# Performance work log

Measured on AMD Instinct MI355X. Metric: run time of the kernel, lower is better.

Reference implementation:

```python
import jax, jax.numpy as jnp
import numpy as np

EPS_SUM = 1e-8
EPS_FILL = 1e-4
NORM_THRESH = 0.1
MASK_THRESH = 0.1


def _shift1(x):
    # conv2d with 1x3 filter [1,1,0], padding (0,1): out[i] = x[i-1] + x[i]
    return x + jnp.pad(x, ((0, 0), (0, 0), (0, 0), (1, 0)))[..., :-1]


def _shift2(x):
    # conv2d with 1x3 filter [0,1,1], padding (0,1): out[i] = x[i] + x[i+1]
    return x + jnp.pad(x, ((0, 0), (0, 0), (0, 0), (0, 1)))[..., 1:]


def _fill(disp, vm, shift_fn, n_steps):
    # Hole filling: each step propagates valid disparity one pixel; after W
    # steps the data-dependent while-loop of the original has converged
    # (further steps are identity), so a fixed-length scan is equivalent.
    def step(carry, _):
        d, m = carry
        m1 = shift_fn(m)
        nm = (m1 > 0).astype(d.dtype)
        d = d * m + shift_fn(d) / (m1 + EPS_FILL) * (nm - m)
        return (d, nm), None
    (disp, vm), _ = jax.lax.scan(step, (disp, vm), None, length=n_steps)
    return disp, vm


def regress_disp(att, valid_mask):
    # att: [B,H,W,W], valid_mask: [B,1,H,W]
    b, h, w, _ = att.shape
    idx = jnp.arange(w, dtype=att.dtype)
    disp_ini = idx[None, None, None, :] - jnp.sum(att * idx, axis=-1).reshape(b, 1, h, w)
    disp = disp_ini * valid_mask
    disp, vm = _fill(disp, valid_mask, _shift1, w)  # left-to-right pass
    disp, vm = _fill(disp, vm, _shift2, w)          # right-to-left pass
    return disp_ini * valid_mask + disp * (1.0 - valid_mask)


def masked_exp_norm(cost, lower):
    # tril/triu-masked exp normalization (non-standard attention)
    tri = jnp.tril if lower else jnp.triu
    c = tri(cost)
    c = jnp.exp(c - jnp.max(c, axis=-1, keepdims=True))
    c = tri(c)
    return c / (jnp.sum(c, axis=-1, keepdims=True) + EPS_SUM)


def gen_pos_shift(w, dtype):
    p = jnp.linspace(0.0, 2.0, w).astype(dtype)
    pos = jnp.maximum(p[:, None] - p[None, :], 0.0)  # pos_l - pos_r, clipped
    return pos[None, None]  # [1,1,W,W]


def gen_raw_disp(att, pos_shift):
    hi = jnp.argmax(att, axis=-1)
    rr = jnp.stack([hi - 1, hi, hi + 1], axis=-1) + 1  # indices into padded axis
    att_pad = jnp.pad(att, ((0, 0), (0, 0), (0, 0), (1, 1)))
    aw = jnp.take_along_axis(att_pad, rr, axis=-1)
    norm = jnp.sum(aw, axis=-1, keepdims=True)
    norm = jnp.where(norm < NORM_THRESH, 1.0, norm)
    aw = aw / norm
    pos_pad = jnp.broadcast_to(jnp.pad(pos_shift, ((0, 0), (0, 0), (0, 0), (1, 1))), att_pad.shape)
    pr = jnp.take_along_axis(pos_pad, rr, axis=-1)
    return jnp.sum(aw * pr, axis=-1)  # [B,H,W]


def setup_inputs() -> dict:
    key = jax.random.key(0)
    k1, k2 = jax.random.split(key)
    B, H, W = 1, 64, 512
    cost1 = jax.random.normal(k1, (B, H, W, W), dtype=jnp.float32)
    cost2 = jax.random.normal(k2, (B, H, W, W), dtype=jnp.float32)
    return {"cost1": cost1, "cost2": cost2}


def reference(cost1, cost2):
    b, h, w, _ = cost1.shape
    att_r2l = masked_exp_norm(cost2, lower=True)   # right-to-left attention
    att_l2r = masked_exp_norm(cost1, lower=False)  # left-to-right attention
    vm_left = (jnp.sum(att_l2r, axis=-2) > MASK_THRESH).astype(cost1.dtype).reshape(b, 1, h, w)
    vm_right = (jnp.sum(att_r2l, axis=-2) > MASK_THRESH).astype(cost1.dtype).reshape(b, 1, h, w)
    disp_r2l = regress_disp(att_r2l, vm_left)   # [B,1,H,W]
    disp_l2r = regress_disp(att_l2r, vm_right)  # [B,1,H,W]
    pos = gen_pos_shift(w, cost1.dtype)
    raw_l2r = gen_raw_disp(att_r2l, pos)                               # [B,H,W]
    raw_r2l = gen_raw_disp(att_l2r, jnp.swapaxes(pos, -1, -2))         # [B,H,W]
    return jnp.concatenate([disp_r2l, disp_l2r, raw_l2r[:, None], raw_r2l[:, None]], axis=1)
```

## Files before the change

kernel.cpp:

```cpp
#include <hip/hip_runtime.h>
#include <float.h>

#define H 64
#define W 512
#define SPLIT 8

template<bool LOWER, bool FULLROW>
__device__ __forceinline__ void process_rows(
    const float* __restrict__ hb, const int h, const int s,
    const int lane, const int wid,
    float* __restrict__ disp, float* __restrict__ raw, float* scol)
{
  constexpr int NH = FULLROW ? 2 : 1;
  constexpr int JB = FULLROW ? 0 : (LOWER ? 0 : 256);
  const float pscale = 2.0f / 511.0f;

  float cacc[NH * 4];
  #pragma unroll
  for (int q = 0; q < NH * 4; q++) cacc[q] = 0.f;

  int   jmap[NH * 4];
  float jfmap[NH * 4];
  #pragma unroll
  for (int hh = 0; hh < NH; hh++)
    #pragma unroll
    for (int k = 0; k < 4; k++) {
      jmap[hh * 4 + k]  = JB + hh * 256 + lane * 4 + k;
      jfmap[hh * 4 + k] = (float)jmap[hh * 4 + k];
    }

  for (int t = wid; t < 64; t += 8) {
    const int i = s * 64 + t;
    const float fi = (float)i;
    const float* rp = hb + (size_t)i * W;

    float c[NH * 4];
    #pragma unroll
    for (int hh = 0; hh < NH; hh++) {
      const float4 v = ((const float4*)rp)[(JB >> 2) + hh * 64 + lane];
      c[hh*4+0] = v.x; c[hh*4+1] = v.y; c[hh*4+2] = v.z; c[hh*4+3] = v.w;
    }

    float best = -FLT_MAX;
    int   bj   = 1024;
    #pragma unroll
    for (int hh = 0; hh < NH; hh++) {
      const bool NM = FULLROW ? (LOWER ? (hh == 1) : (hh == 0)) : true;
      #pragma unroll
      for (int k = 0; k < 4; k++) {
        const int q = hh * 4 + k;
        float v = c[q];
        if (NM) {
          const bool vld = LOWER ? (jmap[q] <= i) : (jmap[q] >= i);
          v = vld ? v : -FLT_MAX;
          c[q] = v;
        }
        if (v > best) { best = v; bj = jmap[q]; }
      }
    }
    #pragma unroll
    for (int off = 32; off; off >>= 1) {
      const float ov = __shfl_xor(best, off);
      const int   oj = __shfl_xor(bj, off);
      if (ov > best || (ov == best && oj < bj)) { best = ov; bj = oj; }
    }

    const int bjm = bj - 1, bjp = bj + 1;
    const int am = min(max(bjm, 0), W - 1);
    const int ap = min(bjp, W - 1);
    const float cm_ = rp[am];
    const float cp_ = rp[ap];

    const bool hasMasked = LOWER ? (i < W - 1) : (i > 0);
    const float mx = hasMasked ? fmaxf(best, 0.f) : best;

    float ssum = 0.f, wsum = 0.f;
    #pragma unroll
    for (int q = 0; q < NH * 4; q++) {
      const float e = __expf(c[q] - mx);
      c[q] = e;
      ssum += e;
      wsum = fmaf(e, jfmap[q], wsum);
    }
    #pragma unroll
    for (int off = 32; off; off >>= 1) {
      ssum += __shfl_xor(ssum, off);
      wsum += __shfl_xor(wsum, off);
    }
    const float inv = 1.f / (ssum + 1e-8f);

    #pragma unroll
    for (int q = 0; q < NH * 4; q++) cacc[q] = fmaf(c[q], inv, cacc[q]);

    if (lane == 0) {
      const bool pv = LOWER ? (bjm >= 0) : (bjm >= i);
      const bool nv = LOWER ? (bjp <= i) : (bjp <= W - 1);
      const float e_h = __expf(best - mx);
      const float e_p = pv ? __expf(cm_ - mx) : 0.f;
      const float e_n = nv ? __expf(cp_ - mx) : 0.f;
      const float t0 = e_p + e_h + e_n;
      const float w0 = fmaf(e_p, (float)bjm, fmaf(e_h, (float)bj, e_n * (float)bjp));
      disp[h * W + i] = fi - wsum * inv;
      const float n0 = t0 * inv;
      const float t1 = pscale * (LOWER ? (fi * t0 - w0) : (w0 - fi * t0));
      raw[h * W + i] = (t1 * inv) / (n0 < 0.1f ? 1.f : n0);
    }
  }

  #pragma unroll
  for (int q = 0; q < NH * 4; q++) atomicAdd(&scol[jmap[q]], cacc[q]);
}

__global__ __launch_bounds__(512) void attn_stats_all(
    const float* __restrict__ cost1, const float* __restrict__ cost2,
    float* __restrict__ disp_r2l, float* __restrict__ disp_l2r,
    float* __restrict__ cs_r2l,  float* __restrict__ cs_l2r,
    float* __restrict__ out)
{
  __shared__ float scol[W];
  const int tid  = threadIdx.x;
  const int lane = tid & 63;
  const int wid  = tid >> 6;
  const int gid  = blockIdx.x;
  const bool lower = (gid & 1) == 0;
  const int rest = gid >> 1;
  const int h    = rest >> 3;
  const int s    = rest & 7;

  const float* cost = lower ? cost2 : cost1;
  float* disp = lower ? disp_r2l : disp_l2r;
  float* csum = lower ? cs_r2l  : cs_l2r;
  float* raw  = out + (lower ? 2 : 3) * (H * W);
  const float* hb = cost + (size_t)h * W * W;

  scol[tid] = 0.f;
  __syncthreads();

  if (lower) {
    if (s < 4) process_rows<true,  false>(hb, h, s, lane, wid, disp, raw, scol);
    else       process_rows<true,  true >(hb, h, s, lane, wid, disp, raw, scol);
  } else {
    if (s < 4) process_rows<false, true >(hb, h, s, lane, wid, disp, raw, scol);
    else       process_rows<false, false>(hb, h, s, lane, wid, disp, raw, scol);
  }
  __syncthreads();

  const bool doMine = lower ? (s >= 4 || tid < 256)
                            : (s < 4  || tid >= 256);
  if (doMine) atomicAdd(&csum[h * W + tid], scol[tid]);
}

__global__ __launch_bounds__(64) void fill_rows(
    const float* __restrict__ dispA, const float* __restrict__ csA,
    const float* __restrict__ dispB, const float* __restrict__ csB,
    float* __restrict__ out)
{
  __shared__ float xrow[W];
  const int pair = blockIdx.x >> 6;
  const int h    = blockIdx.x & 63;
  const float* dsp = (pair ? dispB : dispA) + h * W;
  const float* cs  = (pair ? csB  : csA ) + h * W;
  float* o = out + pair * (H * W) + h * W;
  const int lane = threadIdx.x;
  const int j0 = lane * 8;

  float x[8];
  bool m[8];
  int incl[8];
  int run = -1, fv = W;
  #pragma unroll
  for (int k = 0; k < 8; k++) {
    x[k] = dsp[j0 + k];
    m[k] = cs[j0 + k] > 0.1f;
    xrow[j0 + k] = x[k];
    if (m[k]) { run = j0 + k; if (fv == W) fv = j0 + k; }
    incl[k] = run;
  }
  int v = run;
  #pragma unroll
  for (int off = 1; off < 64; off <<= 1) {
    const int tv = __shfl_up(v, off);
    if (lane >= off) v = max(v, tv);
  }
  int excl = __shfl_up(v, 1);
  if (lane == 0) excl = -1;
  int p0 = fv;
  #pragma unroll
  for (int off = 32; off; off >>= 1) p0 = min(p0, __shfl_xor(p0, off));
  __syncthreads();

  const float C2 = -1.4426229e-4f;
  #pragma unroll
  for (int k = 0; k < 8; k++) {
    const int jj = j0 + k;
    float ov;
    if (m[k]) {
      ov = x[k];
    } else {
      const int p = max(excl, incl[k]);
      if (p >= 0)        ov = xrow[p]  * exp2f(C2 * (float)(jj - p));
      else if (p0 < W)   ov = xrow[p0] * exp2f(C2 * (float)(p0 - jj));
      else               ov = 0.f;
    }
    o[jj] = ov;
  }
}

extern "C" void kernel_launch(void* const* d_in, const int* in_sizes, int n_in,
                              void* d_out, int out_size, void* d_ws, size_t ws_size,
                              hipStream_t stream) {
  const float* cost1 = (const float*)d_in[0];
  const float* cost2 = (const float*)d_in[1];
  float* out = (float*)d_out;
  float* w = (float*)d_ws;
  float* disp_r2l_ini = w;
  float* disp_l2r_ini = w + 32768;
  float* cs_l2r       = w + 65536;
  float* cs_r2l       = w + 98304;

  hipMemsetAsync(cs_l2r, 0, 2 * (size_t)H * W * sizeof(float), stream);

  attn_stats_all<<<2 * H * SPLIT, 512, 0, stream>>>(
      cost1, cost2, disp_r2l_ini, disp_l2r_ini, cs_r2l, cs_l2r, out);

  fill_rows<<<2 * H, 64, 0, stream>>>(disp_r2l_ini, cs_l2r,
                                      disp_l2r_ini, cs_r2l, out);
}
```

Before: 162.2 us.

## Use DPP wave reductions, register neighbor gather, and double block split

Replaces the shuffle-based argmax and sum reductions with DPP row/broadcast steps plus readlane, which avoids LDS-backed cross-lane traffic. The two neighbor values of the argmax are now taken from the already-computed exponentials in registers via readlane, so the dependent global loads and extra exps are gone. It also doubles the row split per image row (SPLIT 16, 32 rows per block) to launch more blocks. In exchange, more blocks each issue their own column-sum atomics, and the select chain adds ALU work.

```diff
diff --git a/kernel.cpp b/kernel.cpp
--- a/kernel.cpp
+++ b/kernel.cpp
@@ -3,7 +3,42 @@
 
 #define H 64
 #define W 512
-#define SPLIT 8
+#define SPLIT 16
+
+
+template<int C>
+__device__ __forceinline__ float dppf(float idv, float v) {
+  return __int_as_float(__builtin_amdgcn_update_dpp(
+      __float_as_int(idv), __float_as_int(v), C, 0xF, 0xF, false));
+}
+template<int C>
+__device__ __forceinline__ int dppi(int idv, int v) {
+  return __builtin_amdgcn_update_dpp(idv, v, C, 0xF, 0xF, false);
+}
+
+__device__ __forceinline__ void argmax_reduce64(float& b, int& j) {
+#define AR_STEP(C) { const float ob = dppf<C>(-FLT_MAX, b); \
+                     const int   oj = dppi<C>(1024, j); \
+                     if (ob > b || (ob == b && oj < j)) { b = ob; j = oj; } }
+  AR_STEP(0x111)
+  AR_STEP(0x112)
+  AR_STEP(0x114)
+  AR_STEP(0x118)
+  AR_STEP(0x142)
+  AR_STEP(0x143)
+#undef AR_STEP
+  b = __int_as_float(__builtin_amdgcn_readlane(__float_as_int(b), 63));
+  j = __builtin_amdgcn_readlane(j, 63);
+}
+
+__device__ __forceinline__ void sum2_reduce64(float& a, float& w) {
+#define S_STEP(C) { a += dppf<C>(0.f, a); w += dppf<C>(0.f, w); }
+  S_STEP(0x111) S_STEP(0x112) S_STEP(0x114) S_STEP(0x118)
+  S_STEP(0x142) S_STEP(0x143)
+#undef S_STEP
+  a = __int_as_float(__builtin_amdgcn_readlane(__float_as_int(a), 63));
+  w = __int_as_float(__builtin_amdgcn_readlane(__float_as_int(w), 63));
+}
 
 template<bool LOWER, bool FULLROW>
 __device__ __forceinline__ void process_rows(
@@ -29,8 +64,8 @@
       jfmap[hh * 4 + k] = (float)jmap[hh * 4 + k];
     }
 
-  for (int t = wid; t < 64; t += 8) {
-    const int i = s * 64 + t;
+  for (int t = wid; t < 32; t += 8) {
+    const int i = s * 32 + t;
     const float fi = (float)i;
     const float* rp = hb + (size_t)i * W;
 
@@ -58,18 +93,7 @@
         if (v > best) { best = v; bj = jmap[q]; }
       }
     }
-    #pragma unroll
-    for (int off = 32; off; off >>= 1) {
-      const float ov = __shfl_xor(best, off);
-      const int   oj = __shfl_xor(bj, off);
-      if (ov > best || (ov == best && oj < bj)) { best = ov; bj = oj; }
-    }
-
-    const int bjm = bj - 1, bjp = bj + 1;
-    const int am = min(max(bjm, 0), W - 1);
-    const int ap = min(bjp, W - 1);
-    const float cm_ = rp[am];
-    const float cp_ = rp[ap];
+    argmax_reduce64(best, bj);
 
     const bool hasMasked = LOWER ? (i < W - 1) : (i > 0);
     const float mx = hasMasked ? fmaxf(best, 0.f) : best;
@@ -82,22 +106,41 @@
       ssum += e;
       wsum = fmaf(e, jfmap[q], wsum);
     }
-    #pragma unroll
-    for (int off = 32; off; off >>= 1) {
-      ssum += __shfl_xor(ssum, off);
-      wsum += __shfl_xor(wsum, off);
-    }
+    sum2_reduce64(ssum, wsum);
     const float inv = 1.f / (ssum + 1e-8f);
 
     #pragma unroll
     for (int q = 0; q < NH * 4; q++) cacc[q] = fmaf(c[q], inv, cacc[q]);
 
+    const int bjm = bj - 1, bjp = bj + 1;
+    const bool pv = LOWER ? (bjm >= 0) : (bjm >= i);
+    const bool nv = LOWER ? (bjp <= i) : (bjp <= W - 1);
+    float e_p = 0.f, e_n = 0.f;
+    {
+      const int jcl = min(max(bjm, JB), JB + NH * 256 - 1);
+      const int rsel = ((jcl - JB) >> 8) * 4 + (jcl & 3);
+      const int lsel = ((jcl - JB) >> 2) & 63;
+      float sel = c[0];
+      #pragma unroll
+      for (int q = 1; q < NH * 4; q++) sel = (rsel == q) ? c[q] : sel;
+      const float g = __int_as_float(
+          __builtin_amdgcn_readlane(__float_as_int(sel), lsel));
+      e_p = pv ? g : 0.f;
+    }
+    {
+      const int jcl = min(max(bjp, JB), JB + NH * 256 - 1);
+      const int rsel = ((jcl - JB) >> 8) * 4 + (jcl & 3);
+      const int lsel = ((jcl - JB) >> 2) & 63;
+      float sel = c[0];
+      #pragma unroll
+      for (int q = 1; q < NH * 4; q++) sel = (rsel == q) ? c[q] : sel;
+      const float g = __int_as_float(
+          __builtin_amdgcn_readlane(__float_as_int(sel), lsel));
+      e_n = nv ? g : 0.f;
+    }
+
     if (lane == 0) {
-      const bool pv = LOWER ? (bjm >= 0) : (bjm >= i);
-      const bool nv = LOWER ? (bjp <= i) : (bjp <= W - 1);
       const float e_h = __expf(best - mx);
-      const float e_p = pv ? __expf(cm_ - mx) : 0.f;
-      const float e_n = nv ? __expf(cp_ - mx) : 0.f;
       const float t0 = e_p + e_h + e_n;
       const float w0 = fmaf(e_p, (float)bjm, fmaf(e_h, (float)bj, e_n * (float)bjp));
       disp[h * W + i] = fi - wsum * inv;
@@ -124,8 +167,8 @@
   const int gid  = blockIdx.x;
   const bool lower = (gid & 1) == 0;
   const int rest = gid >> 1;
-  const int h    = rest >> 3;
-  const int s    = rest & 7;
+  const int h    = rest >> 4;
+  const int s    = rest & 15;
 
   const float* cost = lower ? cost2 : cost1;
   float* disp = lower ? disp_r2l : disp_l2r;
@@ -137,16 +180,16 @@
   __syncthreads();
 
   if (lower) {
-    if (s < 4) process_rows<true,  false>(hb, h, s, lane, wid, disp, raw, scol);
+    if (s < 8) process_rows<true,  false>(hb, h, s, lane, wid, disp, raw, scol);
     else       process_rows<true,  true >(hb, h, s, lane, wid, disp, raw, scol);
   } else {
-    if (s < 4) process_rows<false, true >(hb, h, s, lane, wid, disp, raw, scol);
+    if (s < 8) process_rows<false, true >(hb, h, s, lane, wid, disp, raw, scol);
     else       process_rows<false, false>(hb, h, s, lane, wid, disp, raw, scol);
   }
   __syncthreads();
 
-  const bool doMine = lower ? (s >= 4 || tid < 256)
-                            : (s < 4  || tid >= 256);
+  const bool doMine = lower ? (s >= 8 || tid < 256)
+                            : (s < 8  || tid >= 256);
   if (doMine) atomicAdd(&csum[h * W + tid], scol[tid]);
 }
 
```

Measured after the change: 172.5 us. 1.06x slower.
